# Kernel optimization log

Hardware: AMD Instinct MI355X
Metric: run time of the kernel (lower is better)

The kernel has to match this reference:

```python
import jax, jax.numpy as jnp
import numpy as np

EPS = 1e-5


def spline_conv(x, src, dst, pseudo, W, root, bias, num_nodes, K=5):
    """Degree-1 open B-spline conv (torch_spline_conv semantics), mean aggregation.
    W: [kernel_total, Cin, Cout]. kernel_total==1 means trivial basis (kernel_size=1)."""
    E = src.shape[0]
    Cin = x.shape[1]
    KT = W.shape[0]
    x_j = x[src]                                            # [E, Cin] edge gather
    deg = jax.ops.segment_sum(jnp.ones((E,), x.dtype), dst, num_segments=num_nodes)
    deg = jnp.maximum(deg, 1.0)
    if KT == 1:
        agg = jax.ops.segment_sum(x_j, dst, num_segments=num_nodes)
        out = (agg / deg[:, None]) @ W[0]
    else:
        v = pseudo * (K - 1)                                # open spline: v in [0, K-1]
        f = jnp.clip(jnp.floor(v), 0.0, K - 2)
        frac = v - f                                        # [E, 2]
        fi = f.astype(jnp.int32)
        # bucket basis-weighted source features by (kernel_index, dst) then one dense einsum
        h = jnp.zeros((KT * num_nodes, Cin), x.dtype)
        for s0 in (0, 1):
            for s1 in (0, 1):
                b0 = frac[:, 0] if s0 else 1.0 - frac[:, 0]
                b1 = frac[:, 1] if s1 else 1.0 - frac[:, 1]
                basis = b0 * b1                             # [E]
                wi = (fi[:, 0] + s0) + K * (fi[:, 1] + s1)  # [E] kernel index in [0,25)
                seg = wi * num_nodes + dst
                h = h + jax.ops.segment_sum(basis[:, None] * x_j, seg,
                                            num_segments=KT * num_nodes)
        agg = jnp.einsum('knc,kco->no', h.reshape(KT, num_nodes, Cin), W)
        out = agg / deg[:, None]
    return out + x @ root + bias


def batch_norm(x, gamma, beta):
    m = x.mean(axis=0)
    var = jnp.mean((x - m) ** 2, axis=0)
    return gamma * (x - m) * jax.lax.rsqrt(var + EPS) + beta


def setup_inputs() -> dict:
    key = jax.random.key(0)
    ks = jax.random.split(key, 8)
    N, E, Cin, Cout = 50000, 800000, 32, 64
    x = jax.random.normal(ks[0], (N, Cin), jnp.float32)
    edge_index = jax.random.randint(ks[1], (2, E), 0, N, jnp.int32)
    edge_attr = jax.random.uniform(ks[2], (E, 2), jnp.float32)
    s = 0.1
    return {
        'x': x, 'edge_index': edge_index, 'edge_attr': edge_attr,
        'w1': jax.random.normal(ks[3], (25, Cin, Cout), jnp.float32) * s,
        'r1': jax.random.normal(ks[4], (Cin, Cout), jnp.float32) * s,
        'b1': jnp.zeros((Cout,), jnp.float32),
        'g1': jnp.ones((Cout,), jnp.float32),
        'beta1': jnp.zeros((Cout,), jnp.float32),
        'w2': jax.random.normal(ks[5], (25, Cout, Cout), jnp.float32) * s,
        'r2': jax.random.normal(ks[6], (Cout, Cout), jnp.float32) * s,
        'b2': jnp.zeros((Cout,), jnp.float32),
        'g2': jnp.ones((Cout,), jnp.float32),
        'beta2': jnp.zeros((Cout,), jnp.float32),
        'ws': jax.random.normal(ks[7], (1, Cin, Cout), jnp.float32) * s,
        'rs': jax.random.normal(jax.random.fold_in(key, 99), (Cin, Cout), jnp.float32) * s,
        'bs': jnp.zeros((Cout,), jnp.float32),
        'gs': jnp.ones((Cout,), jnp.float32),
        'betas': jnp.zeros((Cout,), jnp.float32),
    }


def reference(x, edge_index, edge_attr, w1, r1, b1, g1, beta1,
              w2, r2, b2, g2, beta2, ws, rs, bs, gs, betas):
    N = x.shape[0]
    src, dst = edge_index[0], edge_index[1]
    h = jax.nn.elu(batch_norm(spline_conv(x, src, dst, edge_attr, w1, r1, b1, N), g1, beta1))
    left = batch_norm(spline_conv(h, src, dst, edge_attr, w2, r2, b2, N), g2, beta2)
    short = batch_norm(spline_conv(x, src, dst, edge_attr, ws, rs, bs, N), gs, betas)
    return jax.nn.elu(left + short)
```

## Files before the change

kernel.cpp:

```cpp
#include <hip/hip_runtime.h>

#define NN 50000
#define NE 800000
#define DBINS 1024

typedef __attribute__((ext_vector_type(8))) short bf16x8;
typedef __attribute__((ext_vector_type(4))) float f32x4;
typedef __attribute__((ext_vector_type(2))) float f32x2;

__device__ __forceinline__ unsigned short f2bf(float f) {
    union { float f; unsigned u; } v; v.f = f;
    unsigned r = v.u + 0x7FFFu + ((v.u >> 16) & 1u);
    return (unsigned short)(r >> 16);
}

__device__ __forceinline__ int4 ld_ep2(const int4* ep, unsigned idx, int which) {
    return *(const int4*)((const char*)ep + (size_t)(idx * 32u + (unsigned)which * 16u));
}
__device__ __forceinline__ unsigned ld_xu(const unsigned* X, unsigned byteoff) {
    return *(const unsigned*)((const char*)X + (size_t)byteoff);
}

__device__ __forceinline__ f32x2 unpack2(unsigned u) {
    union { unsigned u; float f; } a, b;
    a.u = u << 16;
    b.u = u & 0xFFFF0000u;
    return f32x2{a.f, b.f};
}

__device__ __forceinline__ f32x2 pk_mul_hib(f32x2 w, f32x2 x) {
    f32x2 d;
    asm("v_pk_mul_f32 %0, %1, %2 op_sel:[1,0] op_sel_hi:[1,1]"
        : "=v"(d) : "v"(w), "v"(x));
    return d;
}
__device__ __forceinline__ void pk_fma_lob(f32x2& h, f32x2 w, f32x2 t) {
    asm("v_pk_fma_f32 %0, %1, %2, %0 op_sel:[0,0,0] op_sel_hi:[0,1,1]"
        : "+v"(h) : "v"(w), "v"(t));
}

__device__ __forceinline__ int us_idx(int kk, int r, int m) {
    return kk*544 + (r >> 3)*136 + m*8 + (r & 7);
}

template<bool HS>
__device__ __forceinline__ void edge_acc2(f32x2* h, f32x2& hs,
                                          const int4& pa, const int4& pb, f32x2 x) {
    f32x2 wxy[5];
    wxy[0] = unpack2((unsigned)pa.y);
    wxy[1] = unpack2((unsigned)pa.z);
    wxy[2] = unpack2((unsigned)pa.w);
    wxy[3] = unpack2((unsigned)pb.x);
    wxy[4] = unpack2((unsigned)pb.y);
    if (HS) hs += x;
#pragma unroll
    for (int r1 = 0; r1 < 5; ++r1) {
        f32x2 ty = pk_mul_hib(wxy[r1], x);
#pragma unroll
        for (int r0 = 0; r0 < 5; ++r0)
            pk_fma_lob(h[r1*5 + r0], wxy[r0], ty);
    }
}

__device__ __forceinline__ float eh_reduce(f32x2 v, int eh, int stride) {
    float mine  = eh ? v.y : v.x;
    float other = eh ? v.x : v.y;
    return mine + __shfl_xor(other, stride);
}

__global__ __launch_bounds__(256) void k_zero(int* degi, int* cur, float* stats,
                                              int* dcnt, int* dcur,
                                              unsigned* xz, unsigned* hz) {
    int i = blockIdx.x*256 + threadIdx.x;
    int stride = gridDim.x*256;
    for (int j = i; j < NN; j += stride) { degi[j] = 0; cur[j] = 0; }
    if (i < 384) stats[i] = 0.f;
    if (i < DBINS) { dcnt[i] = 0; dcur[i] = 0; }
    if (i < 16) xz[i] = 0u;
    if (i < 32) hz[i] = 0u;
}

__global__ __launch_bounds__(256) void k_hist(const int* __restrict__ dst, int* degi) {
    int e = blockIdx.x*256 + threadIdx.x;
    if (e < NE) atomicAdd(&degi[dst[e]], 1);
}

__global__ __launch_bounds__(256) void k_scan_block(const int* __restrict__ degi,
                                                    int* off, int* bsum) {
    __shared__ int sh[256];
    int t = threadIdx.x;
    int base = blockIdx.x * 1024;
    int v[4]; int s = 0;
#pragma unroll
    for (int j = 0; j < 4; j++) {
        int idx = base + t*4 + j;
        v[j] = (idx < NN) ? ((degi[idx] + 3) & ~3) : 0;
        s += v[j];
    }
    sh[t] = s; __syncthreads();
    for (int ofs = 1; ofs < 256; ofs <<= 1) {
        int x = (t >= ofs) ? sh[t - ofs] : 0;
        __syncthreads();
        sh[t] += x;
        __syncthreads();
    }
    int ex = sh[t] - s;
#pragma unroll
    for (int j = 0; j < 4; j++) {
        int idx = base + t*4 + j;
        if (idx < NN) off[idx] = ex;
        ex += v[j];
    }
    if (t == 255) bsum[blockIdx.x] = sh[255];
}

__global__ __launch_bounds__(256) void k_dhist(const int* __restrict__ degi, int* dcnt) {
    __shared__ int lh[DBINS];
    int t = threadIdx.x;
#pragma unroll
    for (int j = 0; j < DBINS/256; ++j) lh[t + 256*j] = 0;
    __syncthreads();
    int n = blockIdx.x*256 + t;
    if (n < NN) atomicAdd(&lh[min(degi[n], DBINS-1)], 1);
    __syncthreads();
#pragma unroll
    for (int j = 0; j < DBINS/256; ++j) {
        int b = t + 256*j;
        if (lh[b]) atomicAdd(&dcnt[b], lh[b]);
    }
}

__global__ __launch_bounds__(256) void k_topscan(const int* __restrict__ bsum,
                                                 int* bpre, int nb,
                                                 const int* __restrict__ dcnt,
                                                 int* dbase) {
    __shared__ int sh[256];
    int t = threadIdx.x;
    if (blockIdx.x == 0) {
        int s = (t < nb) ? bsum[t] : 0;
        sh[t] = s; __syncthreads();
        for (int ofs = 1; ofs < 256; ofs <<= 1) {
            int x = (t >= ofs) ? sh[t - ofs] : 0;
            __syncthreads();
            sh[t] += x;
            __syncthreads();
        }
        if (t < nb) bpre[t] = sh[t] - s;
    } else {
        int v[4]; int s = 0;
#pragma unroll
        for (int j = 0; j < 4; j++) { v[j] = dcnt[t*4 + j]; s += v[j]; }
        sh[t] = s; __syncthreads();
        for (int ofs = 1; ofs < 256; ofs <<= 1) {
            int x = (t >= ofs) ? sh[t - ofs] : 0;
            __syncthreads();
            sh[t] += x;
            __syncthreads();
        }
        int ex = sh[t] - s;
#pragma unroll
        for (int j = 0; j < 4; j++) { dbase[t*4 + j] = ex; ex += v[j]; }
    }
}

__global__ __launch_bounds__(256) void k_scan_add(int* off, const int* __restrict__ bpre,
                                                  const int* __restrict__ degi) {
    int i = blockIdx.x*256 + threadIdx.x;
    if (i < NN) {
        int v = off[i] + bpre[i >> 10];
        off[i] = v;
        if (i == NN - 1) off[NN] = v + ((degi[i] + 3) & ~3);
    }
}

__global__ __launch_bounds__(256) void k_pscatter_pad(const int* __restrict__ degi,
                                                      const int* __restrict__ dbase,
                                                      int* dcur, int* perm,
                                                      const int* __restrict__ off,
                                                      int4* __restrict__ ep) {
    __shared__ int lh[DBINS];
    __shared__ int lb[DBINS];
    int t = threadIdx.x;
#pragma unroll
    for (int j = 0; j < DBINS/256; ++j) lh[t + 256*j] = 0;
    __syncthreads();
    int n = blockIdx.x*256 + t;
    int d = 0, lr = 0;
    bool act = (n < NN);
    if (act) {
        d = min(degi[n], DBINS-1);
        lr = atomicAdd(&lh[d], 1);
    }
    __syncthreads();
#pragma unroll
    for (int j = 0; j < DBINS/256; ++j) {
        int b = t + 256*j;
        int c = lh[b];
        lb[b] = c ? atomicAdd(&dcur[b], c) : 0;
    }
    __syncthreads();
    if (act) {
        perm[dbase[d] + lb[d] + lr] = n;
        int base = off[n] + degi[n];
        int end  = off[n + 1];
        for (int p = base; p < end; ++p) {
            ep[2*p]     = make_int4(NN, 0, 0, 0);
            ep[2*p + 1] = make_int4(0, 0, 0, 0);
        }
    }
}

__global__ __launch_bounds__(256) void k_scatter(const int* __restrict__ src,
                                                 const int* __restrict__ dst,
                                                 const float* __restrict__ ea,
                                                 const int* __restrict__ off, int* cur,
                                                 int4* __restrict__ ep) {
    int e = blockIdx.x*256 + threadIdx.x;
    if (e >= NE) return;
    int d = dst[e];
    int p = off[d] + atomicAdd(&cur[d], 1);
    float v0 = ea[2*e]     * 4.f;
    float v1 = ea[2*e + 1] * 4.f;
    unsigned w[5];
#pragma unroll
    for (int r = 0; r < 5; ++r) {
        float wx = fmaxf(1.f - fabsf(v0 - (float)r), 0.f);
        float wy = fmaxf(1.f - fabsf(v1 - (float)r), 0.f);
        w[r] = (unsigned)f2bf(wx) | ((unsigned)f2bf(wy) << 16);
    }
    ep[2*p]     = make_int4(src[e], (int)w[0], (int)w[1], (int)w[2]);
    ep[2*p + 1] = make_int4((int)w[3], (int)w[4], 0, 0);
}

__device__ __forceinline__ void wprep_body(int tid, const float* W, const float* root,
                                           int KTC, unsigned short* Wb) {
    int lane = tid & 63, cot = (tid >> 6) & 3, kk = tid >> 8;
    int co = 16*cot + (lane & 15);
    int kbase = kk*32 + ((lane >> 4) * 8);
    union { unsigned short s[8]; uint4 v; } u;
#pragma unroll
    for (int j = 0; j < 8; j++) {
        int k = kbase + j;
        float val = (k < KTC) ? W[(size_t)k*64 + co] : root[(size_t)(k - KTC)*64 + co];
        u.s[j] = f2bf(val);
    }
    *(uint4*)(Wb + (size_t)tid * 8) = u.v;
}

__global__ __launch_bounds__(256) void k_prep(const float* __restrict__ x,
                                              unsigned short* __restrict__ xb,
                                              const float* __restrict__ w1,
                                              const float* __restrict__ r1,
                                              unsigned short* Wb1,
                                              const float* __restrict__ wsN,
                                              const float* __restrict__ rs,
                                              unsigned short* WbS,
                                              const float* __restrict__ w2,
                                              const float* __restrict__ r2,
                                              unsigned short* Wb2) {
    int b = blockIdx.x, t = threadIdx.x;
    if (b < 1563) {
        int i = b*256 + t;
        if (i >= NN*8) return;
        float4 v = ((const float4*)x)[i];
        uint2 pk;
        pk.x = (unsigned)f2bf(v.x) | ((unsigned)f2bf(v.y) << 16);
        pk.y = (unsigned)f2bf(v.z) | ((unsigned)f2bf(v.w) << 16);
        ((uint2*)xb)[i] = pk;
    } else if (b < 1589) {
        wprep_body((b - 1563)*256 + t, w1, r1, 800, Wb1);
    } else if (b < 1591) {
        wprep_body((b - 1589)*256 + t, wsN, rs, 32, WbS);
    } else {
        wprep_body((b - 1591)*256 + t, w2, r2, 1600, Wb2);
    }
}

__global__ __launch_bounds__(512, 4) void k_conv1s(
        const unsigned* __restrict__ Xbf,
        const int* __restrict__ off,
        const int* __restrict__ degi,
        const int4* __restrict__ ep,
        const int* __restrict__ perm,
        const unsigned short* __restrict__ Wb1,
        const unsigned short* __restrict__ WbS,
        const float* __restrict__ b1,
        const float* __restrict__ bs,
        float* __restrict__ agg1,
        float* __restrict__ aggS) {
    __shared__ __align__(16) unsigned short hb[28*544];
    const int t = threadIdx.x;
    const int g = t >> 5;
    const int q = t & 31;
    const int chp = q & 15;
    const int eh = q >> 4;
    const int n0 = blockIdx.x * 16;
    const int n = perm[n0 + g];

    f32x2 h[25], hs = {0.f, 0.f};
#pragma unroll
    for (int i = 0; i < 25; ++i) h[i] = f32x2{0.f, 0.f};

    const int ebeg = off[n], eend = off[n + 1];
    const float rdeg = 1.f / (float)max(degi[n], 1);

    for (int i = ebeg; i < eend; i += 4) {
        const unsigned i0 = (unsigned)(i + eh), i1 = (unsigned)(i + 2 + eh);
        int4 a0 = ld_ep2(ep, i0, 0), b0 = ld_ep2(ep, i0, 1);
        int4 a1 = ld_ep2(ep, i1, 0), b1 = ld_ep2(ep, i1, 1);
        unsigned u0 = ld_xu(Xbf, (unsigned)a0.x * 64u + (unsigned)chp * 4u);
        unsigned u1 = ld_xu(Xbf, (unsigned)a1.x * 64u + (unsigned)chp * 4u);
        edge_acc2<true>(h, hs, a0, b0, unpack2(u0));
        edge_acc2<true>(h, hs, a1, b1, unpack2(u1));
    }

    const int c = 2*chp + eh;
    const int bw = us_idx(0, c, g);
#pragma unroll
    for (int wi = 0; wi < 25; ++wi)
        hb[wi*544 + bw] = f2bf(eh_reduce(h[wi], eh, 16) * rdeg);
    hb[26*544 + bw] = f2bf(eh_reduce(hs, eh, 16) * rdeg);
    {
        unsigned ux = Xbf[(unsigned)n * 16u + (unsigned)chp];
        unsigned short xb = eh ? (unsigned short)(ux >> 16)
                               : (unsigned short)(ux & 0xFFFFu);
        hb[25*544 + bw] = xb;
        hb[27*544 + bw] = xb;
    }
    __syncthreads();

    const int lane = t & 63, w = t >> 6;
    const int m = lane & 15, qq = lane >> 4;
    const int co = (w & 3)*16 + m;
    const int4 pn = ((const int4*)perm)[(n0 >> 2) + qq];
    const int prow[4] = {pn.x, pn.y, pn.z, pn.w};
    if (w < 4) {
        f32x4 acc = {0.f, 0.f, 0.f, 0.f};
        for (int kk = 0; kk < 26; ++kk) {
            bf16x8 av = *(const bf16x8*)&hb[kk*544 + qq*136 + m*8];
            bf16x8 bv = *(const bf16x8*)(Wb1 + (size_t)((kk*4 + w)*64 + lane) * 8);
            acc = __builtin_amdgcn_mfma_f32_16x16x32_bf16(av, bv, acc, 0, 0, 0);
        }
        const float bb = b1[co];
#pragma unroll
        for (int r = 0; r < 4; ++r)
            agg1[(size_t)prow[r]*64 + co] = acc[r] + bb;
    } else {
        f32x4 accs = {0.f, 0.f, 0.f, 0.f};
#pragma unroll
        for (int s = 0; s < 2; ++s) {
            bf16x8 av = *(const bf16x8*)&hb[(26 + s)*544 + qq*136 + m*8];
            bf16x8 bv = *(const bf16x8*)(WbS + (size_t)((s*4 + (w & 3))*64 + lane) * 8);
            accs = __builtin_amdgcn_mfma_f32_16x16x32_bf16(av, bv, accs, 0, 0, 0);
        }
        const float bb = bs[co];
#pragma unroll
        for (int r = 0; r < 4; ++r)
            aggS[(size_t)prow[r]*64 + co] = accs[r] + bb;
    }
}

__global__ __launch_bounds__(512, 6) void k_conv2(
        const unsigned* __restrict__ Xbf,
        const int* __restrict__ off,
        const int* __restrict__ degi,
        const int4* __restrict__ ep,
        const int* __restrict__ perm,
        const unsigned short* __restrict__ Wb2,
        const float* __restrict__ b2,
        float* __restrict__ agg) {
    __shared__ __align__(16) unsigned short hb[26*544];
    unsigned* hb32 = (unsigned*)hb;
    const int t = threadIdx.x, lane = t & 63, w = t >> 6;
    const int n0 = blockIdx.x * 16;
    const int g = t >> 5;
    const int chp = t & 31;
    const int n = perm[n0 + g];

    f32x2 h[25];
#pragma unroll
    for (int i = 0; i < 25; ++i) h[i] = f32x2{0.f, 0.f};

    const int ebeg = off[n], eend = off[n + 1];
    const float rdeg = 1.f / (float)max(degi[n], 1);

    for (int i = ebeg; i < eend; i += 2) {
        int4 a0 = ld_ep2(ep, (unsigned)i, 0),       b0 = ld_ep2(ep, (unsigned)i, 1);
        int4 a1 = ld_ep2(ep, (unsigned)(i+1), 0),   b1 = ld_ep2(ep, (unsigned)(i+1), 1);
        unsigned u0 = ld_xu(Xbf, (unsigned)a0.x * 128u + (unsigned)chp * 4u);
        unsigned u1 = ld_xu(Xbf, (unsigned)a1.x * 128u + (unsigned)chp * 4u);
        f32x2 dummy = {0.f, 0.f};
        edge_acc2<false>(h, dummy, a0, b0, unpack2(u0));
        edge_acc2<false>(h, dummy, a1, b1, unpack2(u1));
    }

    const int kh = chp >> 4;
    const int r0 = (2*chp) & 31;
    const int dw = us_idx(0, r0, g) >> 1;
#pragma unroll
    for (int wi = 0; wi <= 12; ++wi) {
        unsigned pk = (unsigned)f2bf(h[wi].x * rdeg)
                    | ((unsigned)f2bf(h[wi].y * rdeg) << 16);
        hb32[(unsigned)(2*wi + kh)*272u + dw] = pk;
    }
    __syncthreads();

    const int m = lane & 15, qq = lane >> 4;
    f32x4 acc = {0.f, 0.f, 0.f, 0.f};
    if (w < 4) {
        for (int kk = 0; kk < 26; ++kk) {
            bf16x8 av = *(const bf16x8*)&hb[kk*544 + qq*136 + m*8];
            bf16x8 bv = *(const bf16x8*)(Wb2 + (size_t)((kk*4 + w)*64 + lane) * 8);
            acc = __builtin_amdgcn_mfma_f32_16x16x32_bf16(av, bv, acc, 0, 0, 0);
        }
    }
    __syncthreads();

#pragma unroll
    for (int wi = 13; wi < 25; ++wi) {
        unsigned pk = (unsigned)f2bf(h[wi].x * rdeg)
                    | ((unsigned)f2bf(h[wi].y * rdeg) << 16);
        hb32[(unsigned)(2*wi + kh - 26)*272u + dw] = pk;
    }
    hb32[(unsigned)(24 + kh)*272u + dw] = Xbf[(unsigned)n * 32u + (unsigned)chp];
    __syncthreads();

    if (w >= 4) return;
    for (int kk = 0; kk < 26; ++kk) {
        bf16x8 av = *(const bf16x8*)&hb[kk*544 + qq*136 + m*8];
        bf16x8 bv = *(const bf16x8*)(Wb2 + (size_t)(((kk + 26)*4 + w)*64 + lane) * 8);
        acc = __builtin_amdgcn_mfma_f32_16x16x32_bf16(av, bv, acc, 0, 0, 0);
    }
    const int4 pn = ((const int4*)perm)[(n0 >> 2) + qq];
    const int prow[4] = {pn.x, pn.y, pn.z, pn.w};
    const int co = w*16 + m;
    const float bb = b2[co];
#pragma unroll
    for (int rr = 0; rr < 4; ++rr)
        agg[(size_t)prow[rr]*64 + co] = acc[rr] + bb;
}

__global__ __launch_bounds__(256) void k_bnstats(const float* __restrict__ agg, float* stats) {
    __shared__ float sh0[256], sh1[256];
    int t = threadIdx.x;
    float s = 0.f, ss = 0.f;
    int stride = gridDim.x * 256;
    for (int i = blockIdx.x*256 + t; i < NN*64; i += stride) {
        float v = agg[i];
        s += v; ss += v*v;
    }
    sh0[t] = s; sh1[t] = ss;
    __syncthreads();
    if (t < 64) {
        float a = sh0[t] + sh0[t+64] + sh0[t+128] + sh0[t+192];
        float b = sh1[t] + sh1[t+64] + sh1[t+128] + sh1[t+192];
        atomicAdd(&stats[t], a);
        atomicAdd(&stats[64 + t], b);
    }
}

__global__ __launch_bounds__(256) void k_bnstats2(const float* __restrict__ a1,
                                                  const float* __restrict__ as,
                                                  float* stats) {
    __shared__ float sh0[256], sh1[256];
    int t = threadIdx.x;
    const float* src = (blockIdx.x < 256) ? a1 : as;
    float* dst = (blockIdx.x < 256) ? (stats + 128) : (stats + 256);
    int bid = (blockIdx.x < 256) ? blockIdx.x : blockIdx.x - 256;
    float s = 0.f, ss = 0.f;
    for (int i = bid*256 + t; i < NN*64; i += 256*256) {
        float v = src[i];
        s += v; ss += v*v;
    }
    sh0[t] = s; sh1[t] = ss;
    __syncthreads();
    if (t < 64) {
        float a = sh0[t] + sh0[t+64] + sh0[t+128] + sh0[t+192];
        float b = sh1[t] + sh1[t+64] + sh1[t+128] + sh1[t+192];
        atomicAdd(&dst[t], a);
        atomicAdd(&dst[64 + t], b);
    }
}

__device__ __forceinline__ float eluf(float u) { return u > 0.f ? u : expm1f(u); }

__global__ __launch_bounds__(256) void k_bn_elu(const float* __restrict__ agg,
                                                const float* __restrict__ stats,
                                                const float* __restrict__ gamma,
                                                const float* __restrict__ beta,
                                                unsigned short* __restrict__ outb) {
    int i = blockIdx.x*256 + threadIdx.x;
    if (i >= NN*16) return;
    float4 v = ((const float4*)agg)[i];
    float r[4] = {v.x, v.y, v.z, v.w};
    int c0 = (i << 2) & 63;
#pragma unroll
    for (int j = 0; j < 4; j++) {
        int c = c0 + j;
        float mu = stats[c] * (1.f/NN);
        float var = stats[64 + c] * (1.f/NN) - mu*mu;
        float sc = gamma[c] * rsqrtf(fmaxf(var, 0.f) + 1e-5f);
        r[j] = eluf((r[j] - mu)*sc + beta[c]);
    }
    uint2 pk;
    pk.x = (unsigned)f2bf(r[0]) | ((unsigned)f2bf(r[1]) << 16);
    pk.y = (unsigned)f2bf(r[2]) | ((unsigned)f2bf(r[3]) << 16);
    ((uint2*)outb)[i] = pk;
}

__global__ __launch_bounds__(256) void k_bn_final(const float* __restrict__ a2,
                                                  const float* __restrict__ st2,
                                                  const float* __restrict__ g2,
                                                  const float* __restrict__ be2,
                                                  const float* __restrict__ as,
                                                  const float* __restrict__ sts,
                                                  const float* __restrict__ gs,
                                                  const float* __restrict__ bes,
                                                  float* __restrict__ out) {
    int i = blockIdx.x*256 + threadIdx.x;
    if (i >= NN*16) return;
    float4 v2 = ((const float4*)a2)[i];
    float4 vs = ((const float4*)as)[i];
    float r2v[4] = {v2.x, v2.y, v2.z, v2.w};
    float rsv[4] = {vs.x, vs.y, vs.z, vs.w};
    float o[4];
    int c0 = (i << 2) & 63;
#pragma unroll
    for (int j = 0; j < 4; j++) {
        int c = c0 + j;
        float mu2 = st2[c] * (1.f/NN);
        float var2 = st2[64 + c] * (1.f/NN) - mu2*mu2;
        float sc2 = g2[c] * rsqrtf(fmaxf(var2, 0.f) + 1e-5f);
        float mus = sts[c] * (1.f/NN);
        float vars = sts[64 + c] * (1.f/NN) - mus*mus;
        float scs = gs[c] * rsqrtf(fmaxf(vars, 0.f) + 1e-5f);
        float u = (r2v[j] - mu2)*sc2 + be2[c] + (rsv[j] - mus)*scs + bes[c];
        o[j] = eluf(u);
    }
    ((float4*)out)[i] = make_float4(o[0], o[1], o[2], o[3]);
}

extern "C" void kernel_launch(void* const* d_in, const int* in_sizes, int n_in,
                              void* d_out, int out_size, void* d_ws, size_t ws_size,
                              hipStream_t stream) {
    const float* x   = (const float*)d_in[0];
    const int*   ei  = (const int*)d_in[1];
    const float* ea  = (const float*)d_in[2];
    const float* w1  = (const float*)d_in[3];
    const float* r1  = (const float*)d_in[4];
    const float* b1  = (const float*)d_in[5];
    const float* g1  = (const float*)d_in[6];
    const float* be1 = (const float*)d_in[7];
    const float* w2  = (const float*)d_in[8];
    const float* r2  = (const float*)d_in[9];
    const float* b2  = (const float*)d_in[10];
    const float* g2  = (const float*)d_in[11];
    const float* be2 = (const float*)d_in[12];
    const float* wsN = (const float*)d_in[13];
    const float* rs  = (const float*)d_in[14];
    const float* bs  = (const float*)d_in[15];
    const float* gs  = (const float*)d_in[16];
    const float* bes = (const float*)d_in[17];
    const int* srcp = ei;
    const int* dstp = ei + NE;

    char* wsb = (char*)d_ws;
    size_t o = 0;
    auto alloc = [&](size_t bytes) -> char* {
        char* p = wsb + o;
        o += (bytes + 255) & ~(size_t)255;
        return p;
    };
    int*    degi    = (int*)   alloc((size_t)NN * 4);
    int*    cur     = (int*)   alloc((size_t)NN * 4);
    int*    off     = (int*)   alloc((size_t)(NN + 1) * 4);
    int*    bsum    = (int*)   alloc(256 * 4);
    int*    bpre    = (int*)   alloc(256 * 4);
    int*    dcnt    = (int*)   alloc(DBINS * 4);
    int*    dcur    = (int*)   alloc(DBINS * 4);
    int*    dbase   = (int*)   alloc(DBINS * 4);
    int*    perm    = (int*)   alloc((size_t)NN * 4);
    int4*   ep      = (int4*)  alloc(((size_t)NE + 3*NN + 64) * 32);
    unsigned short* Wb1 = (unsigned short*)alloc(26 * 4096);
    unsigned short* WbS = (unsigned short*)alloc(2 * 4096);
    unsigned short* Wb2 = (unsigned short*)alloc(52 * 4096);
    float*  agg1    = (float*) alloc((size_t)NN * 64 * 4);
    float*  aggS    = (float*) alloc((size_t)NN * 64 * 4);
    unsigned short* h1bf = (unsigned short*)alloc((size_t)(NN + 1) * 64 * 2);
    unsigned short* xbf  = (unsigned short*)alloc((size_t)(NN + 1) * 32 * 2);
    float*  stats   = (float*) alloc(384 * 4);
    (void)ws_size; (void)in_sizes; (void)n_in; (void)out_size;

    float* out = (float*)d_out;

    k_zero<<<196, 256, 0, stream>>>(degi, cur, stats, dcnt, dcur,
                                    (unsigned*)(xbf + (size_t)NN * 32),
                                    (unsigned*)(h1bf + (size_t)NN * 64));
    k_hist<<<3125, 256, 0, stream>>>(dstp, degi);
    k_scan_block<<<49, 256, 0, stream>>>(degi, off, bsum);
    k_dhist<<<196, 256, 0, stream>>>(degi, dcnt);
    k_topscan<<<2, 256, 0, stream>>>(bsum, bpre, 49, dcnt, dbase);
    k_scan_add<<<196, 256, 0, stream>>>(off, bpre, degi);
    k_pscatter_pad<<<196, 256, 0, stream>>>(degi, dbase, dcur, perm, off, ep);
    k_scatter<<<3125, 256, 0, stream>>>(srcp, dstp, ea, off, cur, ep);

    k_prep<<<1643, 256, 0, stream>>>(x, xbf, w1, r1, Wb1, wsN, rs, WbS, w2, r2, Wb2);

    k_conv1s<<<3125, 512, 0, stream>>>((const unsigned*)xbf, off, degi, ep, perm,
                                       Wb1, WbS, b1, bs, agg1, aggS);
    k_bnstats<<<256, 256, 0, stream>>>(agg1, stats);
    k_bn_elu<<<3125, 256, 0, stream>>>(agg1, stats, g1, be1, h1bf);

    k_conv2<<<3125, 512, 0, stream>>>((const unsigned*)h1bf, off, degi, ep, perm,
                                      Wb2, b2, agg1);
    k_bnstats2<<<512, 256, 0, stream>>>(agg1, aggS, stats);
    k_bn_final<<<3125, 256, 0, stream>>>(agg1, stats + 128, g2, be2,
                                         aggS, stats + 256, gs, bes, out);
}
```

Measured before the change: 427.2 us.

## Use sparse 4-tap spline basis in conv2 with compact edge records

Adds a second compact 16-byte edge record holding the source index, the floor-cell selector and the two pairs of linear weights. k_conv2 now accumulates only the 4 nonzero basis products per edge, picked through a wave-uniform switch, instead of a dense 25-tap FMA, and its threads are remapped so each wave handles two nodes at one channel per lane. Both conv kernels now also walk the perm array in reverse, so high-degree nodes start first. The cost is extra scatter writes and memory for the second edge array, and the switch relies on the selector being uniform across each wave (readfirstlane).

```diff
diff --git a/kernel.cpp b/kernel.cpp
--- a/kernel.cpp
+++ b/kernel.cpp
@@ -13,12 +13,21 @@
     unsigned r = v.u + 0x7FFFu + ((v.u >> 16) & 1u);
     return (unsigned short)(r >> 16);
 }
+__device__ __forceinline__ float bf2f(unsigned short s) {
+    union { unsigned u; float f; } q; q.u = (unsigned)s << 16; return q.f;
+}
 
 __device__ __forceinline__ int4 ld_ep2(const int4* ep, unsigned idx, int which) {
     return *(const int4*)((const char*)ep + (size_t)(idx * 32u + (unsigned)which * 16u));
 }
+__device__ __forceinline__ int4 ld_ep1(const int4* ep, unsigned idx) {
+    return *(const int4*)((const char*)ep + (size_t)(idx * 16u));
+}
 __device__ __forceinline__ unsigned ld_xu(const unsigned* X, unsigned byteoff) {
     return *(const unsigned*)((const char*)X + (size_t)byteoff);
+}
+__device__ __forceinline__ unsigned short ld_xh(const unsigned short* X, unsigned byteoff) {
+    return *(const unsigned short*)((const char*)X + (size_t)byteoff);
 }
 
 __device__ __forceinline__ f32x2 unpack2(unsigned u) {
@@ -59,6 +68,25 @@
 #pragma unroll
         for (int r0 = 0; r0 < 5; ++r0)
             pk_fma_lob(h[r1*5 + r0], wxy[r0], ty);
+    }
+}
+
+__device__ __forceinline__ void edge_sparse(float* h, const int4& pa, float x) {
+    f32x2 wx = unpack2((unsigned)pa.z);
+    f32x2 wy = unpack2((unsigned)pa.w);
+    float t0 = x * wy.x, t1 = x * wy.y;
+    int sel = __builtin_amdgcn_readfirstlane(pa.y);
+    switch (sel) {
+#define SPCASE(F1,F0) case F1*4+F0: { \
+        h[F1*5+F0]   = fmaf(wx.x, t0, h[F1*5+F0]); \
+        h[F1*5+F0+1] = fmaf(wx.y, t0, h[F1*5+F0+1]); \
+        h[F1*5+F0+5] = fmaf(wx.x, t1, h[F1*5+F0+5]); \
+        h[F1*5+F0+6] = fmaf(wx.y, t1, h[F1*5+F0+6]); } break;
+        SPCASE(0,0) SPCASE(0,1) SPCASE(0,2) SPCASE(0,3)
+        SPCASE(1,0) SPCASE(1,1) SPCASE(1,2) SPCASE(1,3)
+        SPCASE(2,0) SPCASE(2,1) SPCASE(2,2) SPCASE(2,3)
+        SPCASE(3,0) SPCASE(3,1) SPCASE(3,2) SPCASE(3,3)
+#undef SPCASE
     }
 }
 
@@ -177,7 +205,8 @@
                                                       const int* __restrict__ dbase,
                                                       int* dcur, int* perm,
                                                       const int* __restrict__ off,
-                                                      int4* __restrict__ ep) {
+                                                      int4* __restrict__ epD,
+                                                      int4* __restrict__ epS) {
     __shared__ int lh[DBINS];
     __shared__ int lb[DBINS];
     int t = threadIdx.x;
@@ -204,8 +233,9 @@
         int base = off[n] + degi[n];
         int end  = off[n + 1];
         for (int p = base; p < end; ++p) {
-            ep[2*p]     = make_int4(NN, 0, 0, 0);
-            ep[2*p + 1] = make_int4(0, 0, 0, 0);
+            epD[2*p]     = make_int4(NN, 0, 0, 0);
+            epD[2*p + 1] = make_int4(0, 0, 0, 0);
+            epS[p]       = make_int4(NN, 0, 0, 0);
         }
     }
 }
@@ -214,7 +244,8 @@
                                                  const int* __restrict__ dst,
                                                  const float* __restrict__ ea,
                                                  const int* __restrict__ off, int* cur,
-                                                 int4* __restrict__ ep) {
+                                                 int4* __restrict__ epD,
+                                                 int4* __restrict__ epS) {
     int e = blockIdx.x*256 + threadIdx.x;
     if (e >= NE) return;
     int d = dst[e];
@@ -228,8 +259,15 @@
         float wy = fmaxf(1.f - fabsf(v1 - (float)r), 0.f);
         w[r] = (unsigned)f2bf(wx) | ((unsigned)f2bf(wy) << 16);
     }
-    ep[2*p]     = make_int4(src[e], (int)w[0], (int)w[1], (int)w[2]);
-    ep[2*p + 1] = make_int4((int)w[3], (int)w[4], 0, 0);
+    int s = src[e];
+    epD[2*p]     = make_int4(s, (int)w[0], (int)w[1], (int)w[2]);
+    epD[2*p + 1] = make_int4((int)w[3], (int)w[4], 0, 0);
+    float f0f = fminf(floorf(v0), 3.f), f1f = fminf(floorf(v1), 3.f);
+    float fr0 = v0 - f0f, fr1 = v1 - f1f;
+    int sel = (int)f1f * 4 + (int)f0f;
+    unsigned wp0 = (unsigned)f2bf(1.f - fr0) | ((unsigned)f2bf(fr0) << 16);
+    unsigned wp1 = (unsigned)f2bf(1.f - fr1) | ((unsigned)f2bf(fr1) << 16);
+    epS[p] = make_int4(s, sel, (int)wp0, (int)wp1);
 }
 
 __device__ __forceinline__ void wprep_body(int tid, const float* W, const float* root,
@@ -294,7 +332,7 @@
     const int q = t & 31;
     const int chp = q & 15;
     const int eh = q >> 4;
-    const int n0 = blockIdx.x * 16;
+    const int n0 = NN - 16 - blockIdx.x * 16;
     const int n = perm[n0 + g];
 
     f32x2 h[25], hs = {0.f, 0.f};
@@ -360,48 +398,50 @@
     }
 }
 
+__device__ __forceinline__ void conv2_edges(float* h,
+                                            const unsigned short* __restrict__ Xh,
+                                            const int4* __restrict__ epS,
+                                            int ebeg, int eend, int c) {
+#pragma unroll
+    for (int i = 0; i < 25; ++i) h[i] = 0.f;
+    for (int i = ebeg; i < eend; i += 2) {
+        int4 p0 = ld_ep1(epS, (unsigned)i);
+        int4 p1 = ld_ep1(epS, (unsigned)(i + 1));
+        unsigned short s0 = ld_xh(Xh, (unsigned)p0.x * 128u + (unsigned)c * 2u);
+        unsigned short s1 = ld_xh(Xh, (unsigned)p1.x * 128u + (unsigned)c * 2u);
+        edge_sparse(h, p0, bf2f(s0));
+        edge_sparse(h, p1, bf2f(s1));
+    }
+}
+
 __global__ __launch_bounds__(512, 6) void k_conv2(
-        const unsigned* __restrict__ Xbf,
+        const unsigned short* __restrict__ Xh,
         const int* __restrict__ off,
         const int* __restrict__ degi,
-        const int4* __restrict__ ep,
+        const int4* __restrict__ epS,
         const int* __restrict__ perm,
         const unsigned short* __restrict__ Wb2,
         const float* __restrict__ b2,
         float* __restrict__ agg) {
     __shared__ __align__(16) unsigned short hb[26*544];
-    unsigned* hb32 = (unsigned*)hb;
     const int t = threadIdx.x, lane = t & 63, w = t >> 6;
-    const int n0 = blockIdx.x * 16;
-    const int g = t >> 5;
-    const int chp = t & 31;
-    const int n = perm[n0 + g];
-
-    f32x2 h[25];
-#pragma unroll
-    for (int i = 0; i < 25; ++i) h[i] = f32x2{0.f, 0.f};
-
-    const int ebeg = off[n], eend = off[n + 1];
-    const float rdeg = 1.f / (float)max(degi[n], 1);
-
-    for (int i = ebeg; i < eend; i += 2) {
-        int4 a0 = ld_ep2(ep, (unsigned)i, 0),       b0 = ld_ep2(ep, (unsigned)i, 1);
-        int4 a1 = ld_ep2(ep, (unsigned)(i+1), 0),   b1 = ld_ep2(ep, (unsigned)(i+1), 1);
-        unsigned u0 = ld_xu(Xbf, (unsigned)a0.x * 128u + (unsigned)chp * 4u);
-        unsigned u1 = ld_xu(Xbf, (unsigned)a1.x * 128u + (unsigned)chp * 4u);
-        f32x2 dummy = {0.f, 0.f};
-        edge_acc2<false>(h, dummy, a0, b0, unpack2(u0));
-        edge_acc2<false>(h, dummy, a1, b1, unpack2(u1));
-    }
-
-    const int kh = chp >> 4;
-    const int r0 = (2*chp) & 31;
-    const int dw = us_idx(0, r0, g) >> 1;
+    const int n0 = NN - 16 - blockIdx.x * 16;
+    const int c = lane;
+    const int kh = c >> 5, r = c & 31;
+
+    const int nA = perm[n0 + 2*w], nB = perm[n0 + 2*w + 1];
+    float hA[25], hB[25];
+    conv2_edges(hA, Xh, epS, off[nA], off[nA + 1], c);
+    conv2_edges(hB, Xh, epS, off[nB], off[nB + 1], c);
+    const float rdA = 1.f / (float)max(degi[nA], 1);
+    const float rdB = 1.f / (float)max(degi[nB], 1);
+
+    const int bwA = (r >> 3)*136 + (2*w)*8 + (r & 7);
+    const int bwB = bwA + 8;
 #pragma unroll
     for (int wi = 0; wi <= 12; ++wi) {
-        unsigned pk = (unsigned)f2bf(h[wi].x * rdeg)
-                    | ((unsigned)f2bf(h[wi].y * rdeg) << 16);
-        hb32[(unsigned)(2*wi + kh)*272u + dw] = pk;
+        hb[(2*wi + kh)*544 + bwA] = f2bf(hA[wi] * rdA);
+        hb[(2*wi + kh)*544 + bwB] = f2bf(hB[wi] * rdB);
     }
     __syncthreads();
 
@@ -418,11 +458,11 @@
 
 #pragma unroll
     for (int wi = 13; wi < 25; ++wi) {
-        unsigned pk = (unsigned)f2bf(h[wi].x * rdeg)
-                    | ((unsigned)f2bf(h[wi].y * rdeg) << 16);
-        hb32[(unsigned)(2*wi + kh - 26)*272u + dw] = pk;
-    }
-    hb32[(unsigned)(24 + kh)*272u + dw] = Xbf[(unsigned)n * 32u + (unsigned)chp];
+        hb[(2*wi + kh - 26)*544 + bwA] = f2bf(hA[wi] * rdA);
+        hb[(2*wi + kh - 26)*544 + bwB] = f2bf(hB[wi] * rdB);
+    }
+    hb[(24 + kh)*544 + bwA] = Xh[(unsigned)nA * 64u + (unsigned)c];
+    hb[(24 + kh)*544 + bwB] = Xh[(unsigned)nB * 64u + (unsigned)c];
     __syncthreads();
 
     if (w >= 4) return;
@@ -580,7 +620,8 @@
     int*    dcur    = (int*)   alloc(DBINS * 4);
     int*    dbase   = (int*)   alloc(DBINS * 4);
     int*    perm    = (int*)   alloc((size_t)NN * 4);
-    int4*   ep      = (int4*)  alloc(((size_t)NE + 3*NN + 64) * 32);
+    int4*   epD     = (int4*)  alloc(((size_t)NE + 3*NN + 64) * 32);
+    int4*   epS     = (int4*)  alloc(((size_t)NE + 3*NN + 64) * 16);
     unsigned short* Wb1 = (unsigned short*)alloc(26 * 4096);
     unsigned short* WbS = (unsigned short*)alloc(2 * 4096);
     unsigned short* Wb2 = (unsigned short*)alloc(52 * 4096);
@@ -601,17 +642,17 @@
     k_dhist<<<196, 256, 0, stream>>>(degi, dcnt);
     k_topscan<<<2, 256, 0, stream>>>(bsum, bpre, 49, dcnt, dbase);
     k_scan_add<<<196, 256, 0, stream>>>(off, bpre, degi);
-    k_pscatter_pad<<<196, 256, 0, stream>>>(degi, dbase, dcur, perm, off, ep);
-    k_scatter<<<3125, 256, 0, stream>>>(srcp, dstp, ea, off, cur, ep);
+    k_pscatter_pad<<<196, 256, 0, stream>>>(degi, dbase, dcur, perm, off, epD, epS);
+    k_scatter<<<3125, 256, 0, stream>>>(srcp, dstp, ea, off, cur, epD, epS);
 
     k_prep<<<1643, 256, 0, stream>>>(x, xbf, w1, r1, Wb1, wsN, rs, WbS, w2, r2, Wb2);
 
-    k_conv1s<<<3125, 512, 0, stream>>>((const unsigned*)xbf, off, degi, ep, perm,
+    k_conv1s<<<3125, 512, 0, stream>>>((const unsigned*)xbf, off, degi, epD, perm,
                                        Wb1, WbS, b1, bs, agg1, aggS);
     k_bnstats<<<256, 256, 0, stream>>>(agg1, stats);
     k_bn_elu<<<3125, 256, 0, stream>>>(agg1, stats, g1, be1, h1bf);
 
-    k_conv2<<<3125, 512, 0, stream>>>((const unsigned*)h1bf, off, degi, ep, perm,
+    k_conv2<<<3125, 512, 0, stream>>>(h1bf, off, degi, epS, perm,
                                       Wb2, b2, agg1);
     k_bnstats2<<<512, 256, 0, stream>>>(agg1, aggS, stats);
     k_bn_final<<<3125, 256, 0, stream>>>(agg1, stats + 128, g2, be2,
```

Measured after the change: 610.3 us. 42.9% more time.
